# Optimization experiments

Measured on AMD Instinct MI355X. Metric: run time of the kernel, lower is better.

## Reference

```python
import jax, jax.numpy as jnp
import numpy as np

TAU_MEM = 20.0
TAU_SYN = 5.0
ALPHA_MEM = float(np.exp(-1.0 / TAU_MEM))
ALPHA_SYN = float(np.exp(-1.0 / TAU_SYN))
CONNECTIVITY = 0.1
SPECTRAL_RADIUS = 0.9


def setup_inputs() -> dict:
    key = jax.random.key(0)
    k1, k2, k3, k4 = jax.random.split(key, 4)
    B, D, N = 2048, 256, 512
    rates = jax.random.normal(k1, (B, D), dtype=jnp.float32)
    input_weight = jax.random.normal(k2, (N, D), dtype=jnp.float32) * 0.1
    W = jax.random.normal(k3, (N, N), dtype=jnp.float32)
    mask = (jax.random.uniform(k4, (N, N)) < CONNECTIVITY).astype(jnp.float32)
    W = W * mask
    # mirror torch init: scale by spectral_radius / max eigvalsh
    max_eig = jnp.linalg.eigvalsh(W)[-1]
    W = W * (SPECTRAL_RADIUS / max_eig)
    return {
        "rates": rates,
        "input_weight": input_weight,
        "reservoir_weight": W,
        "v_mem": jnp.zeros((B, N), dtype=jnp.float32),
        "current": jnp.zeros((B, N), dtype=jnp.float32),
        "n_steps": 64,
    }


def reference(rates, input_weight, reservoir_weight, v_mem, current, n_steps):
    dtype = rates.dtype
    # input current is identical every step in the original loop -> hoist it
    input_current = rates @ input_weight.T  # (B, N)

    def step(carry, _):
        v, c, spike_sum = carry
        rec = (c > 0).astype(dtype) @ reservoir_weight  # (B, N)
        c = ALPHA_SYN * c + (1.0 - ALPHA_SYN) * (input_current + rec)
        v = ALPHA_MEM * v + (1.0 - ALPHA_MEM) * c
        spike_sum = spike_sum + (v > 0).astype(dtype)
        return (v, c, spike_sum), None

    (v, c, spike_sum), _ = jax.lax.scan(
        step, (v_mem, current, jnp.zeros_like(v_mem)), None, length=n_steps
    )
    readout = spike_sum / n_steps  # == stack(spikes).mean(dim=1)
    return readout, (v, c)
```

## Files before the change

### kernel.cpp

```cpp
#include <hip/hip_runtime.h>
#include <stdint.h>


#define N_NEU 512
#define B_ROWS 2048
#define D_IN 256
#define R_PB 8
#define NBLK (B_ROWS / R_PB)

#define WS_PERM    0
#define WS_RANK    2048
#define WS_CNT     4096
#define WS_CNTW    8192
#define WS_IBASE   8256
#define WS_WBASE   8320
#define WS_IDX     16384
#define WS_WT      81920

#define SPK_OFF(k)  ((k) << 3)
#define SPK_BUF     4096

__global__ __launch_bounds__(256) void lsm_count(
    const float* __restrict__ W, uint32_t* __restrict__ ws)
{
    int t  = threadIdx.x;
    int k0 = blockIdx.x * 4;
    int c0 = 0, c1 = 0;
    #pragma unroll
    for (int kk = 0; kk < 4; ++kk) {
        const float* row = W + (size_t)(k0 + kk) * N_NEU;
        c0 += (row[t]       != 0.0f) ? 1 : 0;
        c1 += (row[t + 256] != 0.0f) ? 1 : 0;
    }
    if (c0) atomicAdd(&ws[(WS_CNT >> 2) + t],       (uint32_t)c0);
    if (c1) atomicAdd(&ws[(WS_CNT >> 2) + t + 256], (uint32_t)c1);
}

__global__ __launch_bounds__(512) void lsm_sort(uint32_t* __restrict__ ws)
{
    __shared__ int hist[N_NEU + 1];
    __shared__ int csort[N_NEU];
    __shared__ int gcw[8];

    int t = threadIdx.x;
    int creal = (int)ws[(WS_CNT >> 2) + t];
    for (int i = t; i < N_NEU + 1; i += 512) hist[i] = 0;
    __syncthreads();
    atomicAdd(&hist[creal], 1);
    __syncthreads();
    if (t == 0) {
        int acc = 0;
        for (int v = 0; v <= N_NEU; ++v) { int h = hist[v]; hist[v] = acc; acc += h; }
    }
    __syncthreads();
    int rank = atomicAdd(&hist[creal], 1);
    ws[(WS_PERM >> 2) + rank] = (uint32_t)t;
    ws[(WS_RANK >> 2) + t]    = (uint32_t)rank;
    csort[rank] = creal;
    __syncthreads();
    if (t < 8) {
        int cw = csort[t * 64 + 63];
        cw = (cw + 7) & ~7;
        gcw[t] = cw;
        ws[(WS_CNTW >> 2) + t] = (uint32_t)cw;
    }
    __syncthreads();
    if (t == 0) {
        int ai = 0, aw = 0;
        for (int g = 0; g < 8; ++g) {
            ws[(WS_IBASE >> 2) + g] = (uint32_t)ai;
            ws[(WS_WBASE >> 2) + g] = (uint32_t)aw;
            ai += gcw[g] * 64 * 2;
            aw += gcw[g] * 64 * 4;
        }
    }
    __syncthreads();
    int wg = rank >> 6, ls = rank & 63;
    int cw = gcw[wg];
    uint32_t ib = ws[(WS_IBASE >> 2) + wg];
    uint32_t wb = ws[(WS_WBASE >> 2) + wg];
    char* base = (char*)ws;
    for (int j = creal; j < cw; ++j) {
        *(unsigned short*)(base + WS_IDX + ib + (j >> 3) * 1024 + ls * 16 + (j & 7) * 2) = 0;
        *(float*)(base + WS_WT + wb + (j >> 3) * 2048 + ls * 32 + (j & 7) * 4) = 0.0f;
    }
}

__global__ __launch_bounds__(64) void lsm_fill(
    const float* __restrict__ W, uint32_t* __restrict__ ws)
{
    int c    = blockIdx.x;
    int lane = threadIdx.x;
    char* base = (char*)ws;
    uint32_t rank = ws[(WS_RANK >> 2) + c];
    int wg = (int)(rank >> 6), ls = (int)(rank & 63);
    uint32_t ib = ws[(WS_IBASE >> 2) + wg];
    uint32_t wb = ws[(WS_WBASE >> 2) + wg];

    __shared__ int ctr;
    if (lane == 0) ctr = 0;
    __syncthreads();

    for (int k = lane; k < N_NEU; k += 64) {
        float wv = W[(size_t)k * N_NEU + c];
        if (wv != 0.0f) {
            int j = atomicAdd(&ctr, 1);
            *(unsigned short*)(base + WS_IDX + ib + (j >> 3) * 1024 + ls * 16 + (j & 7) * 2)
                = (unsigned short)SPK_OFF(k);
            *(float*)(base + WS_WT + wb + (j >> 3) * 2048 + ls * 32 + (j & 7) * 4) = wv;
        }
    }
}

#define GATH(P, X, B) \
    P##0 = *(const uint2*)((B) + ((X).x & 0xffffu)); \
    P##1 = *(const uint2*)((B) + ((X).x >> 16));     \
    P##2 = *(const uint2*)((B) + ((X).y & 0xffffu)); \
    P##3 = *(const uint2*)((B) + ((X).y >> 16));     \
    P##4 = *(const uint2*)((B) + ((X).z & 0xffffu)); \
    P##5 = *(const uint2*)((B) + ((X).z >> 16));     \
    P##6 = *(const uint2*)((B) + ((X).w & 0xffffu)); \
    P##7 = *(const uint2*)((B) + ((X).w >> 16));

#define C1(S, W) \
    rec0 = fmaf((W), (float)((S).x & 0xffu),         rec0); \
    rec1 = fmaf((W), (float)(((S).x >> 8) & 0xffu),  rec1); \
    rec2 = fmaf((W), (float)(((S).x >> 16) & 0xffu), rec2); \
    rec3 = fmaf((W), (float)((S).x >> 24),           rec3); \
    rec4 = fmaf((W), (float)((S).y & 0xffu),         rec4); \
    rec5 = fmaf((W), (float)(((S).y >> 8) & 0xffu),  rec5); \
    rec6 = fmaf((W), (float)(((S).y >> 16) & 0xffu), rec6); \
    rec7 = fmaf((W), (float)((S).y >> 24),           rec7);

#define CONS(P, WA, WB) \
    C1(P##0, (WA).x) C1(P##1, (WA).y) C1(P##2, (WA).z) C1(P##3, (WA).w) \
    C1(P##4, (WB).x) C1(P##5, (WB).y) C1(P##6, (WB).z) C1(P##7, (WB).w)

#define LDW(WA, WB, K) \
    WA = ((const float4*)(wp0 + (K) * 2048))[0]; \
    WB = ((const float4*)(wp0 + (K) * 2048))[1];

__global__ __launch_bounds__(512, 1)
void lsm_main(
    const float* __restrict__ rates, const float* __restrict__ inW,
    const float* __restrict__ vin,   const float* __restrict__ cin,
    const int* __restrict__ nsteps_p,
    const uint32_t* __restrict__ ws, float* __restrict__ out)
{
    __shared__ __align__(16) unsigned char smem[2 * SPK_BUF + 8192];
    float* rl = (float*)(smem + 2 * SPK_BUF);

    int q    = threadIdx.x;
    int blk  = blockIdx.x;
    int r0   = blk * R_PB;
    int w    = q >> 6;
    int lane = q & 63;
    int wg   = (w < 4) ? w : (11 - w);
    int n    = (int)ws[(WS_PERM >> 2) + wg * 64 + lane];
    int cw   = (int)ws[(WS_CNTW >> 2) + wg];
    int nit  = cw >> 3;
    const char* ip0 = (const char*)ws + WS_IDX + ws[(WS_IBASE >> 2) + wg]
                    + lane * 16;
    const char* wp0 = (const char*)ws + WS_WT  + ws[(WS_WBASE >> 2) + wg]
                    + lane * 32;
    int spk_n = SPK_OFF(n);

    ((float4*)rl)[q] = ((const float4*)(rates + (size_t)r0 * D_IN))[q];
    __syncthreads();

    float I[R_PB] = {0.f, 0.f, 0.f, 0.f, 0.f, 0.f, 0.f, 0.f};
    {
        const float4* wrow = (const float4*)(inW + (size_t)n * D_IN);
        for (int d4 = 0; d4 < D_IN / 4; ++d4) {
            float4 wv = wrow[d4];
            #pragma unroll
            for (int r = 0; r < R_PB; ++r) {
                const float* rr = rl + r * D_IN + d4 * 4;
                I[r] += wv.x * rr[0] + wv.y * rr[1] + wv.z * rr[2] + wv.w * rr[3];
            }
        }
    }

    float c0v[R_PB], v0v[R_PB], ssum[R_PB];
    uint2 sini = make_uint2(0u, 0u);
    #pragma unroll
    for (int r = 0; r < R_PB; ++r) {
        c0v[r] = cin[(size_t)(r0 + r) * N_NEU + n];
        v0v[r] = vin[(size_t)(r0 + r) * N_NEU + n];
        ssum[r] = 0.f;
        unsigned bit = (c0v[r] > 0.f) ? 1u : 0u;
        if (r < 4) sini.x |= bit << (r * 8);
        else       sini.y |= bit << ((r - 4) * 8);
    }
    *(uint2*)(smem + spk_n) = sini;

    uint4 xr0, xr1, xr2, xr3, xr4, xr5, xr6, xr7, xr8, xr9, xr10, xr11;
    const uint4 xz = make_uint4(0u, 0u, 0u, 0u);
    xr0  =              *(const uint4*)(ip0);
    xr1  = (1  < nit) ? *(const uint4*)(ip0 + 1024)  : xz;
    xr2  = (2  < nit) ? *(const uint4*)(ip0 + 2048)  : xz;
    xr3  = (3  < nit) ? *(const uint4*)(ip0 + 3072)  : xz;
    xr4  = (4  < nit) ? *(const uint4*)(ip0 + 4096)  : xz;
    xr5  = (5  < nit) ? *(const uint4*)(ip0 + 5120)  : xz;
    xr6  = (6  < nit) ? *(const uint4*)(ip0 + 6144)  : xz;
    xr7  = (7  < nit) ? *(const uint4*)(ip0 + 7168)  : xz;
    xr8  = (8  < nit) ? *(const uint4*)(ip0 + 8192)  : xz;
    xr9  = (9  < nit) ? *(const uint4*)(ip0 + 9216)  : xz;
    xr10 = (10 < nit) ? *(const uint4*)(ip0 + 10240) : xz;
    xr11 = (11 < nit) ? *(const uint4*)(ip0 + 11264) : xz;

    float4 rw0a, rw0b, rw1a, rw1b, rw2a, rw2b;
    const float4 fz = make_float4(0.f, 0.f, 0.f, 0.f);
    rw0a = ((const float4*)wp0)[0];
    rw0b = ((const float4*)wp0)[1];
    rw1a = (1 < nit) ? ((const float4*)(wp0 + 2048))[0] : fz;
    rw1b = (1 < nit) ? ((const float4*)(wp0 + 2048))[1] : fz;
    rw2a = (2 < nit) ? ((const float4*)(wp0 + 4096))[0] : fz;
    rw2b = (2 < nit) ? ((const float4*)(wp0 + 4096))[1] : fz;

    const float AS   = (float)0.8187307530779818;
    const float OMAS = (float)(1.0 - 0.8187307530779818);
    const float AM   = (float)0.9512294245007140;
    const float OMAM = (float)(1.0 - 0.9512294245007140);

    int T = nsteps_p[0];
    __syncthreads();

    #pragma unroll 1
    for (int t = 0; t < T; ++t) {
        const unsigned char* sb = smem + ((t & 1) ? SPK_BUF : 0);
        unsigned char*       db = smem + ((t & 1) ? 0 : SPK_BUF);

        float rec0 = 0.f, rec1 = 0.f, rec2 = 0.f, rec3 = 0.f;
        float rec4 = 0.f, rec5 = 0.f, rec6 = 0.f, rec7 = 0.f;
        uint2 a0, a1, a2, a3, a4, a5, a6, a7;
        uint2 b0, b1, b2, b3, b4, b5, b6, b7;
        float4 waA, wbA, waB, wbB;

        GATH(a, xr0, sb)
        if (3 < nit) { LDW(waB, wbB, 3) }
        if (1 < nit) { GATH(b, xr1, sb) }
        CONS(a, rw0a, rw0b)
        if (1 < nit) {
            if (2 < nit) { GATH(a, xr2, sb) }
            CONS(b, rw1a, rw1b)
        }
        if (2 < nit) {
            if (3 < nit) { GATH(b, xr3, sb) }
            CONS(a, rw2a, rw2b)
        }
        if (3 < nit) {
            if (4 < nit)  { LDW(waA, wbA, 4)  GATH(a, xr4, sb)  }
            CONS(b, waB, wbB)
        }
        if (4 < nit) {
            if (5 < nit)  { LDW(waB, wbB, 5)  GATH(b, xr5, sb)  }
            CONS(a, waA, wbA)
        }
        if (5 < nit) {
            if (6 < nit)  { LDW(waA, wbA, 6)  GATH(a, xr6, sb)  }
            CONS(b, waB, wbB)
        }
        if (6 < nit) {
            if (7 < nit)  { LDW(waB, wbB, 7)  GATH(b, xr7, sb)  }
            CONS(a, waA, wbA)
        }
        if (7 < nit) {
            if (8 < nit)  { LDW(waA, wbA, 8)  GATH(a, xr8, sb)  }
            CONS(b, waB, wbB)
        }
        if (8 < nit) {
            if (9 < nit)  { LDW(waB, wbB, 9)  GATH(b, xr9, sb)  }
            CONS(a, waA, wbA)
        }
        if (9 < nit) {
            if (10 < nit) { LDW(waA, wbA, 10) GATH(a, xr10, sb) }
            CONS(b, waB, wbB)
        }
        if (10 < nit) {
            if (11 < nit) { LDW(waB, wbB, 11) GATH(b, xr11, sb) }
            CONS(a, waA, wbA)
        }
        if (11 < nit) {
            CONS(b, waB, wbB)
        }

        uint2 ns = make_uint2(0u, 0u);
        {
            float rca[R_PB] = {rec0, rec1, rec2, rec3, rec4, rec5, rec6, rec7};
            #pragma unroll
            for (int r = 0; r < R_PB; ++r) {
                c0v[r] = AS * c0v[r] + OMAS * (I[r] + rca[r]);
                v0v[r] = AM * v0v[r] + OMAM * c0v[r];
                ssum[r] += (v0v[r] > 0.f) ? 1.f : 0.f;
                unsigned bit = (c0v[r] > 0.f) ? 1u : 0u;
                if (r < 4) ns.x |= bit << (r * 8);
                else       ns.y |= bit << ((r - 4) * 8);
            }
        }
        *(uint2*)(db + spk_n) = ns;
        __syncthreads();
    }

    float invT = 1.0f / (float)T;
    size_t BN = (size_t)B_ROWS * N_NEU;
    #pragma unroll
    for (int r = 0; r < R_PB; ++r) {
        size_t off = (size_t)(r0 + r) * N_NEU + n;
        out[off]          = ssum[r] * invT;
        out[BN + off]     = v0v[r];
        out[2 * BN + off] = c0v[r];
    }
}

extern "C" void kernel_launch(void* const* d_in, const int* in_sizes, int n_in,
                              void* d_out, int out_size, void* d_ws, size_t ws_size,
                              hipStream_t stream)
{
    const float* rates = (const float*)d_in[0];
    const float* inW   = (const float*)d_in[1];
    const float* W     = (const float*)d_in[2];
    const float* vin   = (const float*)d_in[3];
    const float* cin   = (const float*)d_in[4];
    const int*   nst   = (const int*)d_in[5];
    uint32_t* ws = (uint32_t*)d_ws;
    float* out = (float*)d_out;
    (void)in_sizes; (void)n_in; (void)out_size; (void)ws_size;

    hipMemsetAsync((char*)d_ws + WS_CNT, 0, 2048, stream);

    lsm_count<<<128, 256, 0, stream>>>(W, ws);
    lsm_sort<<<1, 512, 0, stream>>>(ws);
    lsm_fill<<<N_NEU, 64, 0, stream>>>(W, ws);
    lsm_main<<<NBLK, 512, 0, stream>>>(rates, inW, vin, cin, nst, ws, out);
}
```

Before: 366.7 us.

## Deepen gather/weight pipeline to three stages and coalesce state I/O via LDS

The recurrent sparse-matvec loop moves from a two-deep to a three-deep rotation of spike gathers and weight loads, so more LDS and global loads are in flight ahead of each consume. Initial v/c loads and the final readout/v/c stores now pass through a shared staging buffer, which turns the permuted per-neuron accesses into coalesced row accesses. The cost is more live registers (an extra gather set and weight float4 pair) under a one-block-per-CU bound, plus a larger LDS footprint and several extra barriers in the prologue and epilogue.

Result: slower. 428.6 us (+16.9%).

```diff
diff --git a/kernel.cpp b/kernel.cpp
--- a/kernel.cpp
+++ b/kernel.cpp
@@ -147,8 +147,9 @@
     const int* __restrict__ nsteps_p,
     const uint32_t* __restrict__ ws, float* __restrict__ out)
 {
-    __shared__ __align__(16) unsigned char smem[2 * SPK_BUF + 8192];
-    float* rl = (float*)(smem + 2 * SPK_BUF);
+    __shared__ __align__(16) unsigned char smem[2 * SPK_BUF + 16384];
+    float* stg = (float*)(smem + 2 * SPK_BUF);
+    float* rl  = stg;
 
     int q    = threadIdx.x;
     int blk  = blockIdx.x;
@@ -165,6 +166,22 @@
                     + lane * 32;
     int spk_n = SPK_OFF(n);
 
+    float c0v[R_PB], v0v[R_PB], ssum[R_PB];
+    #pragma unroll
+    for (int r = 0; r < R_PB; ++r)
+        stg[r * N_NEU + q] = cin[(size_t)(r0 + r) * N_NEU + q];
+    __syncthreads();
+    #pragma unroll
+    for (int r = 0; r < R_PB; ++r) c0v[r] = stg[r * N_NEU + n];
+    __syncthreads();
+    #pragma unroll
+    for (int r = 0; r < R_PB; ++r)
+        stg[r * N_NEU + q] = vin[(size_t)(r0 + r) * N_NEU + q];
+    __syncthreads();
+    #pragma unroll
+    for (int r = 0; r < R_PB; ++r) { v0v[r] = stg[r * N_NEU + n]; ssum[r] = 0.f; }
+    __syncthreads();
+
     ((float4*)rl)[q] = ((const float4*)(rates + (size_t)r0 * D_IN))[q];
     __syncthreads();
 
@@ -181,13 +198,9 @@
         }
     }
 
-    float c0v[R_PB], v0v[R_PB], ssum[R_PB];
     uint2 sini = make_uint2(0u, 0u);
     #pragma unroll
     for (int r = 0; r < R_PB; ++r) {
-        c0v[r] = cin[(size_t)(r0 + r) * N_NEU + n];
-        v0v[r] = vin[(size_t)(r0 + r) * N_NEU + n];
-        ssum[r] = 0.f;
         unsigned bit = (c0v[r] > 0.f) ? 1u : 0u;
         if (r < 4) sini.x |= bit << (r * 8);
         else       sini.y |= bit << ((r - 4) * 8);
@@ -233,57 +246,55 @@
 
         float rec0 = 0.f, rec1 = 0.f, rec2 = 0.f, rec3 = 0.f;
         float rec4 = 0.f, rec5 = 0.f, rec6 = 0.f, rec7 = 0.f;
-        uint2 a0, a1, a2, a3, a4, a5, a6, a7;
-        uint2 b0, b1, b2, b3, b4, b5, b6, b7;
-        float4 waA, wbA, waB, wbB;
-
-        GATH(a, xr0, sb)
-        if (3 < nit) { LDW(waB, wbB, 3) }
-        if (1 < nit) { GATH(b, xr1, sb) }
-        CONS(a, rw0a, rw0b)
+        uint2 ga0, ga1, ga2, ga3, ga4, ga5, ga6, ga7;
+        uint2 gb0, gb1, gb2, gb3, gb4, gb5, gb6, gb7;
+        uint2 gc0, gc1, gc2, gc3, gc4, gc5, gc6, gc7;
+        float4 waA, wbA, waB, wbB, waC, wbC;
+
+        GATH(ga, xr0, sb)
+        if (1 < nit) { GATH(gb, xr1, sb) }
+        if (2 < nit) { GATH(gc, xr2, sb) }
+        if (3 < nit) { LDW(waA, wbA, 3) }
+        if (4 < nit) { LDW(waB, wbB, 4) }
+        if (5 < nit) { LDW(waC, wbC, 5) }
+
+        CONS(ga, rw0a, rw0b)
+        if (3 < nit) { GATH(ga, xr3, sb) }
         if (1 < nit) {
-            if (2 < nit) { GATH(a, xr2, sb) }
-            CONS(b, rw1a, rw1b)
+            CONS(gb, rw1a, rw1b)
+            if (4 < nit) { GATH(gb, xr4, sb) }
         }
         if (2 < nit) {
-            if (3 < nit) { GATH(b, xr3, sb) }
-            CONS(a, rw2a, rw2b)
+            CONS(gc, rw2a, rw2b)
+            if (5 < nit) { GATH(gc, xr5, sb) }
         }
         if (3 < nit) {
-            if (4 < nit)  { LDW(waA, wbA, 4)  GATH(a, xr4, sb)  }
-            CONS(b, waB, wbB)
+            CONS(ga, waA, wbA)
+            if (6 < nit) { LDW(waA, wbA, 6) GATH(ga, xr6, sb) }
         }
         if (4 < nit) {
-            if (5 < nit)  { LDW(waB, wbB, 5)  GATH(b, xr5, sb)  }
-            CONS(a, waA, wbA)
+            CONS(gb, waB, wbB)
+            if (7 < nit) { LDW(waB, wbB, 7) GATH(gb, xr7, sb) }
         }
         if (5 < nit) {
-            if (6 < nit)  { LDW(waA, wbA, 6)  GATH(a, xr6, sb)  }
-            CONS(b, waB, wbB)
+            CONS(gc, waC, wbC)
+            if (8 < nit) { LDW(waC, wbC, 8) GATH(gc, xr8, sb) }
         }
         if (6 < nit) {
-            if (7 < nit)  { LDW(waB, wbB, 7)  GATH(b, xr7, sb)  }
-            CONS(a, waA, wbA)
+            CONS(ga, waA, wbA)
+            if (9 < nit) { LDW(waA, wbA, 9) GATH(ga, xr9, sb) }
         }
         if (7 < nit) {
-            if (8 < nit)  { LDW(waA, wbA, 8)  GATH(a, xr8, sb)  }
-            CONS(b, waB, wbB)
+            CONS(gb, waB, wbB)
+            if (10 < nit) { LDW(waB, wbB, 10) GATH(gb, xr10, sb) }
         }
         if (8 < nit) {
-            if (9 < nit)  { LDW(waB, wbB, 9)  GATH(b, xr9, sb)  }
-            CONS(a, waA, wbA)
-        }
-        if (9 < nit) {
-            if (10 < nit) { LDW(waA, wbA, 10) GATH(a, xr10, sb) }
-            CONS(b, waB, wbB)
-        }
-        if (10 < nit) {
-            if (11 < nit) { LDW(waB, wbB, 11) GATH(b, xr11, sb) }
-            CONS(a, waA, wbA)
-        }
-        if (11 < nit) {
-            CONS(b, waB, wbB)
-        }
+            CONS(gc, waC, wbC)
+            if (11 < nit) { LDW(waC, wbC, 11) GATH(gc, xr11, sb) }
+        }
+        if (9 < nit)  { CONS(ga, waA, wbA) }
+        if (10 < nit) { CONS(gb, waB, wbB) }
+        if (11 < nit) { CONS(gc, waC, wbC) }
 
         uint2 ns = make_uint2(0u, 0u);
         {
@@ -304,13 +315,29 @@
 
     float invT = 1.0f / (float)T;
     size_t BN = (size_t)B_ROWS * N_NEU;
-    #pragma unroll
-    for (int r = 0; r < R_PB; ++r) {
-        size_t off = (size_t)(r0 + r) * N_NEU + n;
-        out[off]          = ssum[r] * invT;
-        out[BN + off]     = v0v[r];
-        out[2 * BN + off] = c0v[r];
-    }
+
+    #pragma unroll
+    for (int r = 0; r < R_PB; ++r) stg[r * N_NEU + n] = ssum[r] * invT;
+    __syncthreads();
+    #pragma unroll
+    for (int r = 0; r < R_PB; ++r)
+        out[(size_t)(r0 + r) * N_NEU + q] = stg[r * N_NEU + q];
+    __syncthreads();
+
+    #pragma unroll
+    for (int r = 0; r < R_PB; ++r) stg[r * N_NEU + n] = v0v[r];
+    __syncthreads();
+    #pragma unroll
+    for (int r = 0; r < R_PB; ++r)
+        out[BN + (size_t)(r0 + r) * N_NEU + q] = stg[r * N_NEU + q];
+    __syncthreads();
+
+    #pragma unroll
+    for (int r = 0; r < R_PB; ++r) stg[r * N_NEU + n] = c0v[r];
+    __syncthreads();
+    #pragma unroll
+    for (int r = 0; r < R_PB; ++r)
+        out[2 * BN + (size_t)(r0 + r) * N_NEU + q] = stg[r * N_NEU + q];
 }
 
 extern "C" void kernel_launch(void* const* d_in, const int* in_sizes, int n_in,
```
